# Kernel tuning notes

Measured on AMD Instinct MI355X. Metric: run time of the kernel, lower is better.

## Reference

```python
import jax, jax.numpy as jnp
import numpy as np

LOG2PI = float(np.log(2.0 * np.pi))
B, S, K, D = 64, 512, 64, 16


def setup_inputs() -> dict:
    key = jax.random.key(0)
    k1, k2, k3, k4 = jax.random.split(key, 4)
    z = jax.random.randint(k1, (B, S), 0, K)                       # categorical input
    z_noise = jax.random.normal(k2, (B * S, 1, D), dtype=jnp.float32)  # prior sample z_cont
    t = 0.1 * jax.random.normal(k3, (K, D), dtype=jnp.float32)     # ExtActFixed per-category shift
    log_s = 0.1 * jax.random.normal(k4, (K, D), dtype=jnp.float32) # ExtActFixed per-category log-scale
    return {"z": z, "z_noise": z_noise, "t": t, "log_s": log_s}


def _std_normal_logp(x):
    return -0.5 * x * x - 0.5 * LOG2PI


def reference(z, z_noise, t, log_s):
    b, s = z.shape
    n_cat, d = t.shape
    categ = z.reshape(-1)                                  # [N]
    zc = z_noise                                           # [N,1,D]

    init_log_p = jnp.sum(_std_normal_logp(zc), axis=(1, 2))  # [N]

    # conditional affine flow, forward direction
    t_c = t[categ][:, None, :]                             # gather [N,1,D]
    s_c = log_s[categ][:, None, :]
    z_enc = (zc + t_c) * jnp.exp(s_c)                      # [N,1,D]
    ldj_fwd = jnp.sum(s_c, axis=(1, 2))                    # [N]

    cat_prior = -jnp.log(jnp.float32(n_cat))               # log_softmax(zeros)
    log_point = init_log_p - ldj_fwd + cat_prior           # [N]

    # expand-to-K: inverse flow for every category (broadcast, no explicit tile)
    z_back = z_enc * jnp.exp(-log_s)[None] - t[None]       # [N,K,D]
    back_log_p = jnp.sum(_std_normal_logp(z_back), axis=-1)  # [N,K]
    ldj_back = -jnp.sum(log_s, axis=-1)[None]              # [1,K]
    denom = back_log_p + ldj_back + cat_prior              # [N,K]

    # swap in exact point prob for the true category
    mask = jax.nn.one_hot(categ, n_cat, dtype=denom.dtype) # [N,K]
    denom = denom * (1.0 - mask) + log_point[:, None] * mask
    log_den = jax.nn.logsumexp(denom, axis=-1)             # [N]
    class_prob_log = log_point - log_den                   # [N]

    # beta=1, channel_padding_mask=ones
    ldj_loc = class_prob_log - (init_log_p - ldj_fwd)      # [N]

    z_out = z_enc.reshape(b, s, d)
    ldj = ldj_loc.reshape(b, s).sum(axis=-1)               # [B]
    return z_out, ldj
```

## Files before the change

kernel.cpp:

```cpp
#include <hip/hip_runtime.h>
#include <math.h>

#define NTOT   32768
#define BATCH  64
#define KCAT   64
#define DDIM   16
#define F_LOG2PI 1.8378770664093453f
#define CAT_PRIOR -4.1588830833596715f

constexpr int LPN  = 8;
constexpr int GPN  = 4;
constexpr int BLK  = 256;
constexpr int NPB  = (BLK / LPN) * GPN;
constexpr int NBLK = NTOT / NPB;
constexpr int ROWS = 36;

__global__ __launch_bounds__(BLK) void lce_main(
    const int*   __restrict__ z,
    const float* __restrict__ zn,
    const float* __restrict__ t,
    const float* __restrict__ ls,
    float*       __restrict__ out,
    float*       __restrict__ partial)
{
    __shared__ float comb[KCAT * ROWS];
    __shared__ float est [KCAT * ROWS];
    __shared__ float red[4];

    const int tid = threadIdx.x;

    for (int i = tid; i < KCAT * DDIM; i += BLK) {
        const int k = i >> 4, d = i & 15;
        const float lv = ls[i];
        comb[k * ROWS + d]      = expf(-lv);
        comb[k * ROWS + 16 + d] = t[i];
        est [k * ROWS + d]      = expf(lv);
    }
    if (tid < KCAT) {
        float s = 0.f;
        #pragma unroll
        for (int d = 0; d < DDIM; ++d) s += ls[tid * DDIM + d];
        comb[tid * ROWS + 32] = -0.5f * F_LOG2PI * DDIM - s + CAT_PRIOR;
        comb[tid * ROWS + 33] = s;
    }
    __syncthreads();

    const int q  = tid & (LPN - 1);
    const int n0 = blockIdx.x * NPB + (tid >> 3) * GPN;

    float ze[GPN][DDIM];
    float log_point[GPN], base[GPN];
    int   cat[GPN];

    #pragma unroll
    for (int nn = 0; nn < GPN; ++nn) {
        const int n = n0 + nn;
        const int c = z[n];
        cat[nn] = c;
        const float sumls = comb[c * ROWS + 33];
        const float4* zp = (const float4*)(zn + (long)n * DDIM);
        float ss = 0.f;
        #pragma unroll
        for (int j = 0; j < 4; ++j) {
            const float4 v  = zp[j];
            const float4 tc = *(const float4*)&comb[c * ROWS + 16 + j * 4];
            const float4 ec = *(const float4*)&est [c * ROWS + j * 4];
            ze[nn][j*4+0] = (v.x + tc.x) * ec.x;
            ze[nn][j*4+1] = (v.y + tc.y) * ec.y;
            ze[nn][j*4+2] = (v.z + tc.z) * ec.z;
            ze[nn][j*4+3] = (v.w + tc.w) * ec.w;
            ss = fmaf(v.x, v.x, ss);
            ss = fmaf(v.y, v.y, ss);
            ss = fmaf(v.z, v.z, ss);
            ss = fmaf(v.w, v.w, ss);
        }
        const float init_lp = -0.5f * ss - 8.f * F_LOG2PI;
        base[nn]      = init_lp - sumls;
        log_point[nn] = base[nn] + CAT_PRIOR;
    }

    float dn[GPN][KCAT / LPN];
    float mx[GPN];
    #pragma unroll
    for (int nn = 0; nn < GPN; ++nn) mx[nn] = -1e30f;

    #pragma unroll
    for (int j = 0; j < KCAT / LPN; ++j) {
        const int k = q + j * LPN;
        float is_[DDIM], tr[DDIM];
        #pragma unroll
        for (int jj = 0; jj < 4; ++jj) {
            *(float4*)&is_[jj*4] = *(const float4*)&comb[k * ROWS + jj * 4];
            *(float4*)&tr [jj*4] = *(const float4*)&comb[k * ROWS + 16 + jj * 4];
        }
        const float kc = comb[k * ROWS + 32];
        #pragma unroll
        for (int nn = 0; nn < GPN; ++nn) {
            float acc = 0.f;
            #pragma unroll
            for (int d = 0; d < DDIM; ++d) {
                const float zb = fmaf(ze[nn][d], is_[d], -tr[d]);
                acc = fmaf(zb, zb, acc);
            }
            float dv = fmaf(-0.5f, acc, kc);
            dn[nn][j] = (k == cat[nn]) ? log_point[nn] : dv;
            mx[nn] = fmaxf(mx[nn], dn[nn][j]);
        }
    }

    float ldj_acc = 0.f;
    #pragma unroll
    for (int nn = 0; nn < GPN; ++nn) {
        float m = mx[nn];
        m = fmaxf(m, __shfl_xor(m, 1));
        m = fmaxf(m, __shfl_xor(m, 2));
        m = fmaxf(m, __shfl_xor(m, 4));
        float se = 0.f;
        #pragma unroll
        for (int j = 0; j < KCAT / LPN; ++j) se += __expf(dn[nn][j] - m);
        se += __shfl_xor(se, 1);
        se += __shfl_xor(se, 2);
        se += __shfl_xor(se, 4);
        const float log_den = m + __logf(se);
        ldj_acc += (log_point[nn] - log_den) - base[nn];
    }

    float4* op = (float4*)(out + (long)n0 * DDIM);
#define CH(nn, jj) make_float4(ze[nn][4*(jj)+0], ze[nn][4*(jj)+1], ze[nn][4*(jj)+2], ze[nn][4*(jj)+3])
    switch (q) {
        case 0: op[0] = CH(0,0); op[ 8] = CH(2,0); break;
        case 1: op[1] = CH(0,1); op[ 9] = CH(2,1); break;
        case 2: op[2] = CH(0,2); op[10] = CH(2,2); break;
        case 3: op[3] = CH(0,3); op[11] = CH(2,3); break;
        case 4: op[4] = CH(1,0); op[12] = CH(3,0); break;
        case 5: op[5] = CH(1,1); op[13] = CH(3,1); break;
        case 6: op[6] = CH(1,2); op[14] = CH(3,2); break;
        case 7: op[7] = CH(1,3); op[15] = CH(3,3); break;
    }
#undef CH

    float v = ldj_acc;
    v += __shfl_xor(v, 8);
    v += __shfl_xor(v, 16);
    v += __shfl_xor(v, 32);
    if ((tid & 63) == 0) red[tid >> 6] = v;
    __syncthreads();
    if (tid == 0) partial[blockIdx.x] = red[0] + red[1] + red[2] + red[3];
}

__global__ void lce_fin(const float* __restrict__ partial, float* __restrict__ ldj)
{
    const int b = threadIdx.x;
    if (b < BATCH) {
        float s = 0.f;
        #pragma unroll
        for (int j = 0; j < 4; ++j) s += partial[b * 4 + j];
        ldj[b] = s;
    }
}

extern "C" void kernel_launch(void* const* d_in, const int* in_sizes, int n_in,
                              void* d_out, int out_size, void* d_ws, size_t ws_size,
                              hipStream_t stream)
{
    const int*   z  = (const int*)  d_in[0];
    const float* zn = (const float*)d_in[1];
    const float* t  = (const float*)d_in[2];
    const float* ls = (const float*)d_in[3];
    float* out     = (float*)d_out;
    float* ldj     = out + (long)NTOT * DDIM;
    float* partial = (float*)d_ws;

    lce_main<<<NBLK, BLK, 0, stream>>>(z, zn, t, ls, out, partial);
    lce_fin<<<1, 64, 0, stream>>>(partial, ldj);
}
```

Before: 13.69 us.

## Fuse final batch reduction into main kernel with one block per batch row

Each block now handles a full sequence of 512 points for one batch entry, so the per-batch ldj sum is written directly and the second finalize kernel launch is removed. To make this work, lanes per point drop from 8 to 4 and the block grows to 512 threads. Each lane now evaluates 16 categories instead of 8. The grid shrinks to 64 blocks, which can leave most of the GPU's compute units idle and doubles per-thread work, traded against removing a launch and the partial-sum round trip.

```diff
diff --git a/kernel.cpp b/kernel.cpp
--- a/kernel.cpp
+++ b/kernel.cpp
@@ -3,29 +3,29 @@
 
 #define NTOT   32768
 #define BATCH  64
+#define SEQ    512
 #define KCAT   64
 #define DDIM   16
 #define F_LOG2PI 1.8378770664093453f
 #define CAT_PRIOR -4.1588830833596715f
 
-constexpr int LPN  = 8;
+constexpr int LPN  = 4;
 constexpr int GPN  = 4;
-constexpr int BLK  = 256;
-constexpr int NPB  = (BLK / LPN) * GPN;
-constexpr int NBLK = NTOT / NPB;
+constexpr int BLK  = 512;
+constexpr int NBLK = BATCH;
 constexpr int ROWS = 36;
 
-__global__ __launch_bounds__(BLK) void lce_main(
+__global__ __launch_bounds__(BLK, 2) void lce_fused(
     const int*   __restrict__ z,
     const float* __restrict__ zn,
     const float* __restrict__ t,
     const float* __restrict__ ls,
     float*       __restrict__ out,
-    float*       __restrict__ partial)
+    float*       __restrict__ ldj)
 {
     __shared__ float comb[KCAT * ROWS];
     __shared__ float est [KCAT * ROWS];
-    __shared__ float red[4];
+    __shared__ float red[BLK / 64];
 
     const int tid = threadIdx.x;
 
@@ -46,7 +46,7 @@
     __syncthreads();
 
     const int q  = tid & (LPN - 1);
-    const int n0 = blockIdx.x * NPB + (tid >> 3) * GPN;
+    const int n0 = blockIdx.x * SEQ + (tid >> 2) * GPN;
 
     float ze[GPN][DDIM];
     float log_point[GPN], base[GPN];
@@ -114,13 +114,11 @@
         float m = mx[nn];
         m = fmaxf(m, __shfl_xor(m, 1));
         m = fmaxf(m, __shfl_xor(m, 2));
-        m = fmaxf(m, __shfl_xor(m, 4));
         float se = 0.f;
         #pragma unroll
         for (int j = 0; j < KCAT / LPN; ++j) se += __expf(dn[nn][j] - m);
         se += __shfl_xor(se, 1);
         se += __shfl_xor(se, 2);
-        se += __shfl_xor(se, 4);
         const float log_den = m + __logf(se);
         ldj_acc += (log_point[nn] - log_den) - base[nn];
     }
@@ -128,34 +126,25 @@
     float4* op = (float4*)(out + (long)n0 * DDIM);
 #define CH(nn, jj) make_float4(ze[nn][4*(jj)+0], ze[nn][4*(jj)+1], ze[nn][4*(jj)+2], ze[nn][4*(jj)+3])
     switch (q) {
-        case 0: op[0] = CH(0,0); op[ 8] = CH(2,0); break;
-        case 1: op[1] = CH(0,1); op[ 9] = CH(2,1); break;
-        case 2: op[2] = CH(0,2); op[10] = CH(2,2); break;
-        case 3: op[3] = CH(0,3); op[11] = CH(2,3); break;
-        case 4: op[4] = CH(1,0); op[12] = CH(3,0); break;
-        case 5: op[5] = CH(1,1); op[13] = CH(3,1); break;
-        case 6: op[6] = CH(1,2); op[14] = CH(3,2); break;
-        case 7: op[7] = CH(1,3); op[15] = CH(3,3); break;
+        case 0: op[ 0] = CH(0,0); op[ 4] = CH(1,0); op[ 8] = CH(2,0); op[12] = CH(3,0); break;
+        case 1: op[ 1] = CH(0,1); op[ 5] = CH(1,1); op[ 9] = CH(2,1); op[13] = CH(3,1); break;
+        case 2: op[ 2] = CH(0,2); op[ 6] = CH(1,2); op[10] = CH(2,2); op[14] = CH(3,2); break;
+        case 3: op[ 3] = CH(0,3); op[ 7] = CH(1,3); op[11] = CH(2,3); op[15] = CH(3,3); break;
     }
 #undef CH
 
     float v = ldj_acc;
+    v += __shfl_xor(v, 4);
     v += __shfl_xor(v, 8);
     v += __shfl_xor(v, 16);
     v += __shfl_xor(v, 32);
     if ((tid & 63) == 0) red[tid >> 6] = v;
     __syncthreads();
-    if (tid == 0) partial[blockIdx.x] = red[0] + red[1] + red[2] + red[3];
-}
-
-__global__ void lce_fin(const float* __restrict__ partial, float* __restrict__ ldj)
-{
-    const int b = threadIdx.x;
-    if (b < BATCH) {
-        float s = 0.f;
+    if (tid == 0) {
+        float s = red[0];
         #pragma unroll
-        for (int j = 0; j < 4; ++j) s += partial[b * 4 + j];
-        ldj[b] = s;
+        for (int w = 1; w < BLK / 64; ++w) s += red[w];
+        ldj[blockIdx.x] = s;
     }
 }
 
@@ -167,10 +156,8 @@
     const float* zn = (const float*)d_in[1];
     const float* t  = (const float*)d_in[2];
     const float* ls = (const float*)d_in[3];
-    float* out     = (float*)d_out;
-    float* ldj     = out + (long)NTOT * DDIM;
-    float* partial = (float*)d_ws;
+    float* out = (float*)d_out;
+    float* ldj = out + (long)NTOT * DDIM;
 
-    lce_main<<<NBLK, BLK, 0, stream>>>(z, zn, t, ls, out, partial);
-    lce_fin<<<1, 64, 0, stream>>>(partial, ldj);
+    lce_fused<<<NBLK, BLK, 0, stream>>>(z, zn, t, ls, out, ldj);
 }
```

Result: slower. 18.38 us (+34.3%).
